# Optimization experiments

Measured on AMD Instinct MI355X. Metric: run time of the kernel, lower is better.

The kernel has to match this reference:

```python
import jax, jax.numpy as jnp
import numpy as np

N = 50000
E = 800000
IN_CH = 64
OUT_CH = 64
K = 2  # kernel_size (dim=1, degree=1 B-spline -> linear interpolation)


def setup_inputs() -> dict:
    key = jax.random.key(0)
    k1, k2, k3, k4, k5, k6 = jax.random.split(key, 6)
    x = jax.random.normal(k1, (N, IN_CH), dtype=jnp.float32)
    edge_index = jax.random.randint(k2, (2, E), 0, N, dtype=jnp.int64)
    edge_attr = jax.random.uniform(k3, (E, 1), dtype=jnp.float32)  # pseudo coords in [0,1]
    scale = 1.0 / np.sqrt(IN_CH)
    weight = jax.random.normal(k4, (K, IN_CH, OUT_CH), dtype=jnp.float32) * scale
    root = jax.random.normal(k5, (IN_CH, OUT_CH), dtype=jnp.float32) * scale
    bias = jax.random.normal(k6, (OUT_CH,), dtype=jnp.float32) * 0.01
    return {"x": x, "edge_index": edge_index, "edge_attr": edge_attr,
            "weight": weight, "root": root, "bias": bias}


def reference(x, edge_index, edge_attr, weight, root, bias):
    # SplineConv, dim=1, kernel_size=2, degree=1, open spline, aggr='mean',
    # root_weight=True, bias=True. Followed by ReLU; dropout is identity (eval mode).
    src, dst = edge_index[0], edge_index[1]
    u = edge_attr[:, 0]                      # [E], pseudo in [0,1]
    v = u * (K - 1)
    i0 = jnp.clip(jnp.floor(v).astype(jnp.int32), 0, K - 1)
    i1 = jnp.clip(i0 + 1, 0, K - 1)
    f = v - jnp.floor(v)                     # fractional part -> linear basis (1-f, f)
    # Precompute x @ W_k for each kernel index: [K, N, OUT]
    xw = jnp.einsum('ni,kio->kno', x, weight)
    # Per-edge weighted message: [E, OUT]
    m = (1.0 - f)[:, None] * xw[i0, src] + f[:, None] * xw[i1, src]
    # Mean aggregation at target nodes
    agg = jax.ops.segment_sum(m, dst, num_segments=N)
    cnt = jax.ops.segment_sum(jnp.ones((E,), dtype=x.dtype), dst, num_segments=N)
    out = agg / jnp.maximum(cnt, 1.0)[:, None]
    out = out + x @ root + bias
    return jax.nn.relu(out)
```

## Files before the change

kernel.cpp:

```cpp
#include <hip/hip_runtime.h>
#include <hip/hip_bf16.h>
#include <hip/hip_fp16.h>

#define CH 64
#define BSHIFT 7
#define BINSZ 128
#define BCAP 3072
#define EPB 4096
#define MAXBINS 400

typedef _Float16 f16x8 __attribute__((ext_vector_type(8)));
typedef float f32x4 __attribute__((ext_vector_type(4)));
typedef float f32x2 __attribute__((ext_vector_type(2)));

__global__ __launch_bounds__(256) void prepw_kernel(
        const float* __restrict__ w,
        const float* __restrict__ root,
        _Float16* __restrict__ WT,
        int* __restrict__ bin_cursor, int n_bins) {
    const int t = threadIdx.x;
    if (blockIdx.x == 0)
        for (int i = t; i < n_bins; i += 256) bin_cursor[i] = 0;
    const int gt = blockIdx.x * 256 + t;
    for (int id = gt; id < 192 * 8; id += 2048) {
        int n = id >> 3, c = id & 7;
        const float* src = (n < 128) ? (w + (n >> 6) * 4096 + (n & 63))
                                     : (root + (n - 128));
        f16x8 v;
#pragma unroll
        for (int j = 0; j < 8; ++j) v[j] = (_Float16)src[(c * 8 + j) * 64];
        *(f16x8*)(WT + n * 64 + c * 8) = v;
    }
}

__device__ __forceinline__ void mfma_body(
        int bb, const float* __restrict__ x, const _Float16* __restrict__ WT,
        const float* __restrict__ bias, unsigned short* __restrict__ xwp,
        __half* __restrict__ base, int n_nodes) {
    const int wave = threadIdx.x >> 6, lane = threadIdx.x & 63;
    const int m0 = bb * 64 + wave * 16;
    const int c = lane & 15, g = lane >> 4;
    int arow = m0 + c; if (arow > n_nodes - 1) arow = n_nodes - 1;
    const float* xr = x + (size_t)arow * CH + g * 8;
    f32x4 v0 = *(const f32x4*)(xr);
    f32x4 v1 = *(const f32x4*)(xr + 4);
    f32x4 v2 = *(const f32x4*)(xr + 32);
    f32x4 v3 = *(const f32x4*)(xr + 36);
    f16x8 a0, a1;
#pragma unroll
    for (int j = 0; j < 4; ++j) {
        a0[j] = (_Float16)v0[j]; a0[4 + j] = (_Float16)v1[j];
        a1[j] = (_Float16)v2[j]; a1[4 + j] = (_Float16)v3[j];
    }
    f32x4 acc[12];
#pragma unroll
    for (int nt = 0; nt < 12; ++nt) acc[nt] = (f32x4){0.f, 0.f, 0.f, 0.f};
#pragma unroll
    for (int nt = 0; nt < 12; ++nt) {
        int n = nt * 16 + c;
        f16x8 b0 = *(const f16x8*)(WT + n * 64 + g * 8);
        f16x8 b1 = *(const f16x8*)(WT + n * 64 + 32 + g * 8);
        acc[nt] = __builtin_amdgcn_mfma_f32_16x16x32_f16(a0, b0, acc[nt], 0, 0, 0);
        acc[nt] = __builtin_amdgcn_mfma_f32_16x16x32_f16(a1, b1, acc[nt], 0, 0, 0);
    }
    float bv[4];
#pragma unroll
    for (int gr = 0; gr < 4; ++gr) bv[gr] = bias[gr * 16 + c];
#pragma unroll
    for (int reg = 0; reg < 4; ++reg) {
        int node = m0 + g * 4 + reg;
        if (node < n_nodes) {
#pragma unroll
            for (int gr = 0; gr < 4; ++gr) {
                int ch = gr * 16 + c;
                int pk = __builtin_amdgcn_cvt_pk_fp8_f32(
                    acc[gr][reg], acc[gr + 4][reg], 0, false);
                xwp[(size_t)node * CH + ch] = (unsigned short)(pk & 0xFFFF);
                base[(size_t)node * CH + ch] = __float2half(acc[gr + 8][reg] + bv[gr]);
            }
        }
    }
}

__global__ __launch_bounds__(256) void fused_kernel(
        const float* __restrict__ x, const _Float16* __restrict__ WT,
        const float* __restrict__ bias,
        const int* __restrict__ ei, const float* __restrict__ ea,
        int* __restrict__ bin_cursor, unsigned int* __restrict__ binned,
        unsigned short* __restrict__ xwp, __half* __restrict__ base,
        int n_nodes, int n_edges, int n_bins, int part_blocks) {
    __shared__ uint2 sh[EPB];
    __shared__ int hist[MAXBINS], bstart[MAXBINS + 1];
    __shared__ int gbase[MAXBINS], lcur[MAXBINS];
    if (blockIdx.x >= part_blocks) {
        mfma_body(blockIdx.x - part_blocks, x, WT, bias, xwp, base, n_nodes);
        return;
    }
    const int t = threadIdx.x;
    for (int i = t; i < n_bins; i += 256) hist[i] = 0;
    __syncthreads();
    const int e0 = blockIdx.x * EPB;
    uint2 rec[EPB / 256];
#pragma unroll
    for (int k = 0; k < EPB / 256; ++k) {
        int e = e0 + k * 256 + t;
        if (e < n_edges) {
            int s = ei[e];
            int d = ei[n_edges + e];
            float u = ea[e];
            float fl = floorf(u);
            int i0 = max(0, min((int)fl, 1));
            int i1 = min(i0 + 1, 1);
            float f = u - fl;
            float a1 = ((i0 == 1) ? (1.f - f) : 0.f) + ((i1 == 1) ? f : 0.f);
            unsigned q = __float2uint_rn(a1 * 255.f);
            unsigned dloc = (unsigned)(d & (BINSZ - 1));
            rec[k] = make_uint2((unsigned)s | (q << 16) | (dloc << 24), (unsigned)d);
            atomicAdd(&hist[d >> BSHIFT], 1);
        } else {
            rec[k] = make_uint2(0u, 0xFFFFFFFFu);
        }
    }
    __syncthreads();
    if (t < 64) {
        int carry = 0;
        for (int b = 0; b < n_bins; b += 64) {
            int i = b + t;
            int v = (i < n_bins) ? hist[i] : 0;
            int incl = v;
#pragma unroll
            for (int off = 1; off < 64; off <<= 1) {
                int nv = __shfl_up(incl, off);
                if (t >= off) incl += nv;
            }
            if (i < n_bins) bstart[i] = incl - v + carry;
            carry += __shfl(incl, 63);
        }
        if (t == 0) bstart[n_bins] = carry;
    }
    __syncthreads();
    for (int i = t; i < n_bins; i += 256) {
        int cnt = hist[i];
        gbase[i] = cnt ? atomicAdd(&bin_cursor[i], cnt) : 0;
        lcur[i] = bstart[i];
    }
    __syncthreads();
#pragma unroll
    for (int k = 0; k < EPB / 256; ++k) {
        if (rec[k].y != 0xFFFFFFFFu) {
            int b = (int)(rec[k].y >> BSHIFT);
            int p = atomicAdd(&lcur[b], 1);
            sh[p] = rec[k];
        }
    }
    __syncthreads();
    int total = bstart[n_bins];
    for (int idx = t; idx < total; idx += 256) {
        uint2 r = sh[idx];
        int b = (int)(r.y >> BSHIFT);
        int loc = gbase[b] + (idx - bstart[b]);
        if (loc < BCAP) binned[(size_t)b * BCAP + loc] = r.x;
    }
}

__global__ __launch_bounds__(1024) void gatherbin_kernel(
        const unsigned int* __restrict__ binned,
        const int* __restrict__ bin_count,
        const unsigned short* __restrict__ xwp,
        const __half* __restrict__ base,
        float* __restrict__ out,
        int n_nodes) {
    __shared__ unsigned int raw[BCAP];
    __shared__ unsigned int scsr[BCAP];
    __shared__ int dcnt[BINSZ], dbase[BINSZ], dcur[BINSZ];
    const int bin = blockIdx.x;
    const int t = threadIdx.x;
    int cnt = bin_count[bin]; if (cnt > BCAP) cnt = BCAP;
    if (t < BINSZ) dcnt[t] = 0;
    __syncthreads();
    for (int i = t; i < cnt; i += 1024) {
        unsigned r = binned[(size_t)bin * BCAP + i];
        raw[i] = r;
        atomicAdd(&dcnt[r >> 24], 1);
    }
    __syncthreads();
    if (t < 64) {
        int carry = 0;
        for (int b = 0; b < BINSZ; b += 64) {
            int i = b + t;
            int v = dcnt[i];
            int incl = v;
#pragma unroll
            for (int off = 1; off < 64; off <<= 1) {
                int nv = __shfl_up(incl, off);
                if (t >= off) incl += nv;
            }
            dbase[i] = incl - v + carry;
            carry += __shfl(incl, 63);
        }
    }
    __syncthreads();
    if (t < BINSZ) dcur[t] = dbase[t];
    __syncthreads();
    for (int i = t; i < cnt; i += 1024) {
        unsigned r = raw[i];
        int p = atomicAdd(&dcur[r >> 24], 1);
        scsr[p] = r & 0x00FFFFFFu;
    }
    __syncthreads();
    const int wave = t >> 6, lane = t & 63;
    const float qs = 1.f / 255.f;
    for (int dl = wave; dl < BINSZ; dl += 16) {
        int node = (bin << BSHIFT) + dl;
        if (node >= n_nodes) continue;
        int deg = dcnt[dl];
        int beg = dbase[dl], end = beg + deg;
        float acc = 0.f;
        for (int tb = beg; tb < end; tb += 64) {
            int n = end - tb; if (n > 64) n = 64;
            int r = 0;
            if (lane < n) r = (int)scsr[tb + lane];
            int j = 0;
            for (; j + 4 <= n; j += 4) {
                int p0 = __shfl(r, j),     p1 = __shfl(r, j + 1);
                int p2 = __shfl(r, j + 2), p3 = __shfl(r, j + 3);
                float u0 = (float)(((unsigned)p0 >> 16) & 255u) * qs;
                float u1 = (float)(((unsigned)p1 >> 16) & 255u) * qs;
                float u2 = (float)(((unsigned)p2 >> 16) & 255u) * qs;
                float u3 = (float)(((unsigned)p3 >> 16) & 255u) * qs;
                f32x2 a = __builtin_amdgcn_cvt_pk_f32_fp8(
                    (int)xwp[(size_t)(p0 & 0xFFFF) * CH + lane], false);
                f32x2 b = __builtin_amdgcn_cvt_pk_f32_fp8(
                    (int)xwp[(size_t)(p1 & 0xFFFF) * CH + lane], false);
                f32x2 c = __builtin_amdgcn_cvt_pk_f32_fp8(
                    (int)xwp[(size_t)(p2 & 0xFFFF) * CH + lane], false);
                f32x2 d = __builtin_amdgcn_cvt_pk_f32_fp8(
                    (int)xwp[(size_t)(p3 & 0xFFFF) * CH + lane], false);
                acc += fmaf(u0, a[1] - a[0], a[0]);
                acc += fmaf(u1, b[1] - b[0], b[0]);
                acc += fmaf(u2, c[1] - c[0], c[0]);
                acc += fmaf(u3, d[1] - d[0], d[0]);
            }
            for (; j < n; ++j) {
                int p0 = __shfl(r, j);
                float u0 = (float)(((unsigned)p0 >> 16) & 255u) * qs;
                f32x2 a = __builtin_amdgcn_cvt_pk_f32_fp8(
                    (int)xwp[(size_t)(p0 & 0xFFFF) * CH + lane], false);
                acc += fmaf(u0, a[1] - a[0], a[0]);
            }
        }
        float c = (float)(deg > 0 ? deg : 1);
        size_t o = (size_t)node * CH + lane;
        out[o] = fmaxf(acc / c + __half2float(base[o]), 0.f);
    }
}

extern "C" void kernel_launch(void* const* d_in, const int* in_sizes, int n_in,
                              void* d_out, int out_size, void* d_ws, size_t ws_size,
                              hipStream_t stream) {
    const float* x    = (const float*)d_in[0];
    const int*   ei   = (const int*)d_in[1];
    const float* ea   = (const float*)d_in[2];
    const float* w    = (const float*)d_in[3];
    const float* root = (const float*)d_in[4];
    const float* bias = (const float*)d_in[5];
    float* out = (float*)d_out;

    const int n_nodes = in_sizes[0] / CH;
    const int n_edges = in_sizes[2];
    const int n_bins  = (n_nodes + BINSZ - 1) >> BSHIFT;
    const int part_blocks = (n_edges + EPB - 1) / EPB;
    const int mfma_blocks = (n_nodes + 63) / 64;

    unsigned short* xwp  = (unsigned short*)d_ws;
    __half*       base   = (__half*)(xwp + (size_t)n_nodes * CH);
    unsigned int* binned = (unsigned int*)(base + (size_t)n_nodes * CH);
    _Float16*     WT     = (_Float16*)(binned + (size_t)n_bins * BCAP);
    int*          bin_cursor = (int*)(WT + 192 * 64);

    prepw_kernel<<<8, 256, 0, stream>>>(w, root, WT, bin_cursor, n_bins);
    fused_kernel<<<part_blocks + mfma_blocks, 256, 0, stream>>>(
        x, WT, bias, ei, ea, bin_cursor, binned, xwp, base,
        n_nodes, n_edges, n_bins, part_blocks);
    gatherbin_kernel<<<n_bins, 1024, 0, stream>>>(binned, bin_cursor, xwp,
                                                  base, out, n_nodes);
}
```

Measured before the change: 64.77 us.

## Split each gather bin across two half-bin blocks of 512 threads

The gather kernel now launches two blocks per destination bin. Each block covers 64 of the 128 nodes, builds a local CSR only for its half, and uses 512 threads instead of 1024. The aim is more, smaller blocks to improve occupancy and load balance across CUs, given only about 391 bins. In exchange, both halves re-read the whole bin from global memory and filter it, and a new per-half cap of 2048 edges could drop edges if a half is overfull.

```diff
diff --git a/kernel.cpp b/kernel.cpp
--- a/kernel.cpp
+++ b/kernel.cpp
@@ -6,6 +6,7 @@
 #define BSHIFT 7
 #define BINSZ 128
 #define BCAP 3072
+#define HCAP 2048
 #define EPB 4096
 #define MAXBINS 400
 
@@ -163,7 +164,7 @@
     }
 }
 
-__global__ __launch_bounds__(1024) void gatherbin_kernel(
+__global__ __launch_bounds__(512) void gatherbin_kernel(
         const unsigned int* __restrict__ binned,
         const int* __restrict__ bin_count,
         const unsigned short* __restrict__ xwp,
@@ -171,50 +172,50 @@
         float* __restrict__ out,
         int n_nodes) {
     __shared__ unsigned int raw[BCAP];
-    __shared__ unsigned int scsr[BCAP];
-    __shared__ int dcnt[BINSZ], dbase[BINSZ], dcur[BINSZ];
-    const int bin = blockIdx.x;
+    __shared__ unsigned int scsr[HCAP];
+    __shared__ int dcnt[64], dbase[64], dcur[64];
+    const int bin = blockIdx.x >> 1;
+    const int half = blockIdx.x & 1;
     const int t = threadIdx.x;
     int cnt = bin_count[bin]; if (cnt > BCAP) cnt = BCAP;
-    if (t < BINSZ) dcnt[t] = 0;
-    __syncthreads();
-    for (int i = t; i < cnt; i += 1024) {
+    if (t < 64) dcnt[t] = 0;
+    __syncthreads();
+    for (int i = t; i < cnt; i += 512) {
         unsigned r = binned[(size_t)bin * BCAP + i];
         raw[i] = r;
-        atomicAdd(&dcnt[r >> 24], 1);
+        int dl = (int)(r >> 24);
+        if ((dl >> 6) == half) atomicAdd(&dcnt[dl & 63], 1);
     }
     __syncthreads();
     if (t < 64) {
-        int carry = 0;
-        for (int b = 0; b < BINSZ; b += 64) {
-            int i = b + t;
-            int v = dcnt[i];
-            int incl = v;
-#pragma unroll
-            for (int off = 1; off < 64; off <<= 1) {
-                int nv = __shfl_up(incl, off);
-                if (t >= off) incl += nv;
-            }
-            dbase[i] = incl - v + carry;
-            carry += __shfl(incl, 63);
-        }
-    }
-    __syncthreads();
-    if (t < BINSZ) dcur[t] = dbase[t];
-    __syncthreads();
-    for (int i = t; i < cnt; i += 1024) {
+        int v = dcnt[t];
+        int incl = v;
+#pragma unroll
+        for (int off = 1; off < 64; off <<= 1) {
+            int nv = __shfl_up(incl, off);
+            if (t >= off) incl += nv;
+        }
+        dbase[t] = incl - v;
+        dcur[t] = incl - v;
+    }
+    __syncthreads();
+    for (int i = t; i < cnt; i += 512) {
         unsigned r = raw[i];
-        int p = atomicAdd(&dcur[r >> 24], 1);
-        scsr[p] = r & 0x00FFFFFFu;
+        int dl = (int)(r >> 24);
+        if ((dl >> 6) == half) {
+            int p = atomicAdd(&dcur[dl & 63], 1);
+            if (p < HCAP) scsr[p] = r & 0x00FFFFFFu;
+        }
     }
     __syncthreads();
     const int wave = t >> 6, lane = t & 63;
     const float qs = 1.f / 255.f;
-    for (int dl = wave; dl < BINSZ; dl += 16) {
-        int node = (bin << BSHIFT) + dl;
+    for (int dl = wave; dl < 64; dl += 8) {
+        int node = (bin << BSHIFT) + half * 64 + dl;
         if (node >= n_nodes) continue;
         int deg = dcnt[dl];
         int beg = dbase[dl], end = beg + deg;
+        if (end > HCAP) end = HCAP;
         float acc = 0.f;
         for (int tb = beg; tb < end; tb += 64) {
             int n = end - tb; if (n > 64) n = 64;
@@ -282,6 +283,6 @@
     fused_kernel<<<part_blocks + mfma_blocks, 256, 0, stream>>>(
         x, WT, bias, ei, ea, bin_cursor, binned, xwp, base,
         n_nodes, n_edges, n_bins, part_blocks);
-    gatherbin_kernel<<<n_bins, 1024, 0, stream>>>(binned, bin_cursor, xwp,
-                                                  base, out, n_nodes);
-}
+    gatherbin_kernel<<<2 * n_bins, 512, 0, stream>>>(binned, bin_cursor, xwp,
+                                                     base, out, n_nodes);
+}
```

After: 64.28 us. No clear change (-0.8%).
